# Kernel tuning notes

Measured on AMD Instinct MI355X. Metric: run time of the kernel, lower is better.

Reference implementation:

```python
import jax, jax.numpy as jnp
import numpy as np
from jax import lax

DECAY = 0.1
THRESH = 0.5
LENS = 1.0
D_IN = 2 * 34 * 34  # 2312
HID = 800
NC = 10

@jax.custom_vjp
def act_fun(x):
    return (x > THRESH).astype(x.dtype)

def _act_fwd(x):
    return act_fun(x), x

def _act_bwd(x, g):
    p = jax.nn.sigmoid((x - THRESH) / LENS)
    return (g * p * (1.0 - p) / LENS,)

act_fun.defvjp(_act_fwd, _act_bwd)


def setup_inputs() -> dict:
    key = jax.random.key(0)
    ks = jax.random.split(key, 8)
    B, T = 128, 300
    inp = jax.random.uniform(ks[0], (B, 2, 34, 34, 50), dtype=jnp.float32)
    X = jnp.zeros((B, 2, 34, 34, T), dtype=jnp.float32)
    idx = jax.random.randint(ks[1], (B,), 0, T - 50)
    W1 = jax.random.normal(ks[2], (HID, D_IN), dtype=jnp.float32) * 0.02
    b1 = jnp.zeros((HID,), dtype=jnp.float32)
    W2 = jax.random.normal(ks[3], (NC, HID), dtype=jnp.float32) * 0.03
    b2 = jnp.zeros((NC,), dtype=jnp.float32)
    Wc = jax.random.uniform(ks[4], (1, HID + 4), dtype=jnp.float32)  # ctrl init U(0,1)
    bc = jax.random.uniform(ks[5], (1,), dtype=jnp.float32)
    return {"input": inp, "X": X, "idx": idx, "W1": W1, "b1": b1,
            "W2": W2, "b2": b2, "Wc": Wc, "bc": bc}


def _paste(Xi, clip_i, idx_i):
    # X[i, :, :, :, idx:idx+50] = input[i].view(2,34,34,50)
    return lax.dynamic_update_slice(Xi, clip_i, (0, 0, 0, idx_i))


def reference(input, X, idx, W1, b1, W2, b2, Wc, bc):
    B = X.shape[0]
    T = X.shape[-1]
    X = jax.vmap(_paste)(X, input, idx.astype(jnp.int32))
    xs = jnp.moveaxis(X.reshape(B, D_IN, T), -1, 0)  # [T, B, D_IN]

    t = jnp.arange(T)
    freqs = jnp.stack([
        jnp.ones(T), (t % 2 == 0).astype(jnp.float32),
        (t % 10 == 0).astype(jnp.float32), (t % 100 == 0).astype(jnp.float32),
    ], axis=1).astype(X.dtype)  # [T, 4]
    is_first = (t == 0)

    f32 = X.dtype
    carry0 = (
        jnp.zeros((B, HID), f32), jnp.zeros((B, HID), f32),   # h1_mem, h1_spike
        jnp.zeros((B, NC), f32), jnp.zeros((B, NC), f32),     # h2_mem, h2_spike
        jnp.zeros((B, 1), f32), jnp.zeros((B, 1), f32),       # c_mem, c_spike
        jnp.ones((B, 1), f32), jnp.zeros((B, NC), f32),       # bgt, h2_sumspike
    )

    def step(carry, inps):
        h1m, h1s, h2m, h2s, cm, cs, bgt, sum2 = carry
        x, fq, first = inps
        x_a = jnp.where(first, x, x * cs)
        bgt = jnp.where(cs == 1.0, bgt + 1.0, bgt)
        h1m = h1m * DECAY * (1.0 - h1s) + x_a @ W1.T + b1
        h1s = act_fun(h1m)
        h2m = h2m * DECAY * (1.0 - h2s) + h1s @ W2.T + b2
        h2s = act_fun(h2m)
        c_in = jnp.concatenate(
            [lax.stop_gradient(h1s), jnp.broadcast_to(fq, (B, 4))], axis=1)
        cm = cm * 0.1 * (1.0 - cs) + c_in @ Wc.T + bc
        cs = act_fun(cm)
        sum2 = sum2 + h2s
        return (h1m, h1s, h2m, h2s, cm, cs, bgt, sum2), None

    carry, _ = lax.scan(step, carry0, (xs, freqs, is_first))
    bgt, sum2 = carry[6], carry[7]
    rate = sum2 / bgt
    return rate, X
```

## Files before the change

### kernel.cpp

```cpp
#include <hip/hip_runtime.h>

#define D_IN 2312
#define HID  800
#define NCLS 10
#define BATCH 128
#define TSTEPS 300
#define WIN  50

#define MT 64
#define NT 32
#define BKK 16
#define NTM 100
#define NTN 25
#define GEMM_BLOCKS (NTM * NTN)
#define BLK 128
#define RPASTE 1920
#define TOTQ (BATCH * D_IN * (TSTEPS / 4))

__global__ __launch_bounds__(BLK) void gemm_kernel(
    const float* __restrict__ inp,
    const float* __restrict__ W1,
    float*       __restrict__ P)
{
  __shared__ float As[BKK][MT];
  __shared__ float Bs[BKK][NT + 4];

  int t   = threadIdx.x;
  int bx0 = blockIdx.x;

  int xcd = bx0 & 7;
  int jj  = bx0 >> 3;
  const int q8 = GEMM_BLOCKS >> 3;
  const int r8 = GEMM_BLOCKS & 7;
  int bx = (xcd < r8 ? xcd * (q8 + 1) : r8 * (q8 + 1) + (xcd - r8) * q8) + jj;

  int mt = bx / NTN;
  int nt = bx - mt * NTN;
  int m0 = mt * MT, n0 = nt * NT;

  int am = t & 63;
  int ah = t >> 6;
  int r  = m0 + am;
  int bb = r / 50, ss = r - bb * 50;
  const float* aptr = inp + (size_t)bb * (D_IN * WIN) + ss;

  int bn = t >> 4;
  int bk = t & 15;

  int l  = t & 63;
  int lm = l & 7;
  int ln = l >> 3;
  int tm = ah * 32 + lm * 4;
  int tn = ln * 4;

  float aN[8], bN[4];
#pragma unroll
  for (int q = 0; q < 8; ++q) aN[q] = aptr[(ah * 8 + q) * WIN];
#pragma unroll
  for (int p = 0; p < 4; ++p)
    bN[p] = W1[(size_t)(n0 + bn + 8 * p) * D_IN + bk];

  float acc[4][4] = {};

  for (int k0 = 0; k0 < D_IN; k0 += BKK) {
#pragma unroll
    for (int q = 0; q < 8; ++q) As[ah * 8 + q][am] = aN[q];
#pragma unroll
    for (int p = 0; p < 4; ++p) Bs[bk][bn + 8 * p] = bN[p];
    __syncthreads();

    int kn0 = k0 + BKK;
    if (kn0 + BKK <= D_IN) {
#pragma unroll
      for (int q = 0; q < 8; ++q) aN[q] = aptr[(kn0 + ah * 8 + q) * WIN];
#pragma unroll
      for (int p = 0; p < 4; ++p)
        bN[p] = W1[(size_t)(n0 + bn + 8 * p) * D_IN + kn0 + bk];
    } else if (kn0 < D_IN) {
#pragma unroll
      for (int q = 0; q < 8; ++q) {
        int kk = kn0 + ah * 8 + q;
        aN[q] = (kk < D_IN) ? aptr[kk * WIN] : 0.f;
      }
#pragma unroll
      for (int p = 0; p < 4; ++p) {
        int kk = kn0 + bk;
        bN[p] = (kk < D_IN) ? W1[(size_t)(n0 + bn + 8 * p) * D_IN + kk] : 0.f;
      }
    }

#pragma unroll
    for (int kk = 0; kk < BKK; ++kk) {
      float4 A0 = *(const float4*)&As[kk][tm];
      float4 B0 = *(const float4*)&Bs[kk][tn];
      float av[4] = {A0.x, A0.y, A0.z, A0.w};
      float bv[4] = {B0.x, B0.y, B0.z, B0.w};
#pragma unroll
      for (int i = 0; i < 4; ++i)
#pragma unroll
        for (int j = 0; j < 4; ++j)
          acc[i][j] += av[i] * bv[j];
    }
    __syncthreads();
  }

#pragma unroll
  for (int i = 0; i < 4; ++i) {
    int row = m0 + tm + i;
    *(float4*)&P[(size_t)row * HID + n0 + tn] =
        make_float4(acc[i][0], acc[i][1], acc[i][2], acc[i][3]);
  }
}

template <int CTRL>
__device__ __forceinline__ float dpp_add(float s) {
  return s + __int_as_float(__builtin_amdgcn_update_dpp(
      0, __float_as_int(s), CTRL, 0xf, 0xf, true));
}
__device__ __forceinline__ float wave_sum(float s) {
  s = dpp_add<0x111>(s);
  s = dpp_add<0x112>(s);
  s = dpp_add<0x114>(s);
  s = dpp_add<0x118>(s);
  s = dpp_add<0x142>(s);
  s = dpp_add<0x143>(s);
  return __int_as_float(__builtin_amdgcn_readlane(__float_as_int(s), 63));
}

__global__ __launch_bounds__(64, 1) void recur_kernel(
    const float* __restrict__ P,
    const float* __restrict__ W2,
    const float* __restrict__ b2,
    const float* __restrict__ Wc,
    const float* __restrict__ bc,
    const float* __restrict__ b1,
    const int*   __restrict__ idx,
    float*       __restrict__ out,
    const float* __restrict__ inp,
    float*       __restrict__ outX)
{
  int L = threadIdx.x;
  int b = blockIdx.x;

  if (b >= BATCH) {
    int tid = (b - BATCH) * 64 + L;
    const int stride = RPASTE * 64;
    for (int i = tid; i < TOTQ; i += stride) {
      int q  = i % 75;
      int rd = i / 75;
      int bb = rd / D_IN;
      int d  = rd - bb * D_IN;
      int ib = idx[bb];
      const float* ip = inp + (size_t)bb * (D_IN * WIN) + (size_t)d * WIN;
      int t0 = q * 4;
      float v[4];
#pragma unroll
      for (int e = 0; e < 4; ++e) {
        unsigned w = (unsigned)(t0 + e - ib);
        v[e] = (w < (unsigned)WIN) ? ip[w] : 0.f;
      }
      *(float4*)&outX[(size_t)rd * TSTEPS + t0] = make_float4(v[0], v[1], v[2], v[3]);
    }
    return;
  }

  int myidx = idx[b];
  const float* Pb = P + (size_t)b * WIN * HID;

  float m[13], b1r[13], wcr[13];
  float w2r[NCLS][13];
  unsigned smask = 0;
#pragma unroll
  for (int rr = 0; rr < 13; ++rr) {
    int j = L + 64 * rr;
    bool ok = (j < HID);
    m[rr]   = 0.f;
    b1r[rr] = ok ? b1[j] : 0.f;
    wcr[rr] = ok ? Wc[j] : 0.f;
#pragma unroll
    for (int c = 0; c < NCLS; ++c)
      w2r[c][rr] = ok ? W2[c * HID + j] : 0.f;
  }

  float cm = 0.f, cs = 0.f, bgt = 1.f;
  float bc0 = bc[0];
  float wf0 = Wc[HID], wf1 = Wc[HID + 1], wf2 = Wc[HID + 2], wf3 = Wc[HID + 3];

  float h2m[10], h2s[10], sum2[10], b2r[10];
#pragma unroll
  for (int c = 0; c < NCLS; ++c) { h2m[c] = 0.f; h2s[c] = 0.f; sum2[c] = 0.f; b2r[c] = b2[c]; }

  float cur[13];
  {
    unsigned w0 = (unsigned)(0 - myidx);
    if (w0 < (unsigned)WIN) {
      const float* Pr = Pb + (size_t)w0 * HID;
#pragma unroll
      for (int rr = 0; rr < 13; ++rr) {
        int j = L + 64 * rr;
        cur[rr] = (j < HID) ? Pr[j] : 0.f;
      }
    } else {
#pragma unroll
      for (int rr = 0; rr < 13; ++rr) cur[rr] = 0.f;
    }
  }

  for (int step = 0; step < TSTEPS; ++step) {
    float gate = (step == 0) ? 1.f : cs;

    float nxt[13];
    {
      unsigned wn = (unsigned)(step + 1 - myidx);
      if (wn < (unsigned)WIN) {
        const float* Pr = Pb + (size_t)wn * HID;
#pragma unroll
        for (int rr = 0; rr < 13; ++rr) {
          int j = L + 64 * rr;
          nxt[rr] = (j < HID) ? Pr[j] : 0.f;
        }
      } else {
#pragma unroll
        for (int rr = 0; rr < 13; ++rr) nxt[rr] = 0.f;
      }
    }

    unsigned nmask = 0;
#pragma unroll
    for (int rr = 0; rr < 13; ++rr) {
      float mprev = ((smask >> rr) & 1u) ? 0.f : m[rr] * 0.1f;
      float mv = mprev + cur[rr] * gate + b1r[rr];
      m[rr] = mv;
      nmask |= (mv > 0.5f) ? (1u << rr) : 0u;
    }
    smask = nmask;

    unsigned long long ball = __ballot(smask != 0u);

    float ctrl = 0.f;
    float dot[10];
#pragma unroll
    for (int c = 0; c < NCLS; ++c) dot[c] = 0.f;

    if (ball) {
      float cacc = 0.f;
#pragma unroll
      for (int rr = 0; rr < 13; ++rr) {
        float f = (float)((smask >> rr) & 1u);
        cacc = fmaf(f, wcr[rr], cacc);
      }
      ctrl = wave_sum(cacc);

#pragma unroll
      for (int rr = 0; rr < 13; ++rr) {
        float f = (float)((smask >> rr) & 1u);
#pragma unroll
        for (int c = 0; c < NCLS; ++c)
          dot[c] = fmaf(f, w2r[c][rr], dot[c]);
      }
#pragma unroll
      for (int c = 0; c < NCLS; ++c) dot[c] = wave_sum(dot[c]);
    }

    bgt += (cs == 1.f) ? 1.f : 0.f;
    float fq = wf0;
    if ((step & 1) == 0)   fq += wf1;
    if (step % 10 == 0)    fq += wf2;
    if (step % 100 == 0)   fq += wf3;
    float cv = (cs != 0.f ? 0.f : cm * 0.1f) + ctrl + fq + bc0;
    cm = cv;
    cs = (cv > 0.5f) ? 1.f : 0.f;

#pragma unroll
    for (int c = 0; c < NCLS; ++c) {
      float v = (h2s[c] != 0.f ? 0.f : h2m[c] * 0.1f) + dot[c] + b2r[c];
      h2m[c] = v;
      h2s[c] = (v > 0.5f) ? 1.f : 0.f;
      sum2[c] += h2s[c];
    }

#pragma unroll
    for (int rr = 0; rr < 13; ++rr) cur[rr] = nxt[rr];
  }

  if (L == 0) {
#pragma unroll
    for (int c = 0; c < NCLS; ++c) out[b * NCLS + c] = sum2[c] / bgt;
  }
}

extern "C" void kernel_launch(void* const* d_in, const int* in_sizes, int n_in,
                              void* d_out, int out_size, void* d_ws, size_t ws_size,
                              hipStream_t stream) {
  const float* inp = (const float*)d_in[0];
  const int*   idx = (const int*)d_in[2];
  const float* W1  = (const float*)d_in[3];
  const float* b1  = (const float*)d_in[4];
  const float* W2  = (const float*)d_in[5];
  const float* b2  = (const float*)d_in[6];
  const float* Wc  = (const float*)d_in[7];
  const float* bc  = (const float*)d_in[8];

  float* out = (float*)d_out;
  float* P   = (float*)d_ws;

  gemm_kernel<<<GEMM_BLOCKS, BLK, 0, stream>>>(inp, W1, P);

  recur_kernel<<<BATCH + RPASTE, 64, 0, stream>>>(
      P, W2, b2, Wc, bc, b1, idx, out, inp, out + BATCH * NCLS);
}
```

Before: 1.015 ms.

## Fuse GEMM, recurrence and paste into one kernel with per-tile completion counters

Merges the W1 GEMM, the per-batch spiking recurrence and the X paste into one launch. GEMM blocks bump a per-M-tile atomic counter when done, and each recurrence block spin-waits only on the tiles covering its 50 rows, so recurrence can start before the whole GEMM finishes and the paste overlaps both. The recurrence blocks now read W2 from global memory each step instead of holding it in registers, presumably to cut register pressure under the shared 128-thread launch bound. This risks deadlock if waiting blocks starve GEMM blocks of slots, adds per-step W2 load traffic, and needs extra workspace for the counters, with the old two-kernel path kept as a fallback.

```diff
diff --git a/kernel.cpp b/kernel.cpp
--- a/kernel.cpp
+++ b/kernel.cpp
@@ -14,103 +14,11 @@
 #define NTN 25
 #define GEMM_BLOCKS (NTM * NTN)
 #define BLK 128
-#define RPASTE 1920
+#define RPASTE 960
+#define PASTE_BASE (GEMM_BLOCKS + BATCH)
+#define NB (PASTE_BASE + RPASTE)
 #define TOTQ (BATCH * D_IN * (TSTEPS / 4))
-
-__global__ __launch_bounds__(BLK) void gemm_kernel(
-    const float* __restrict__ inp,
-    const float* __restrict__ W1,
-    float*       __restrict__ P)
-{
-  __shared__ float As[BKK][MT];
-  __shared__ float Bs[BKK][NT + 4];
-
-  int t   = threadIdx.x;
-  int bx0 = blockIdx.x;
-
-  int xcd = bx0 & 7;
-  int jj  = bx0 >> 3;
-  const int q8 = GEMM_BLOCKS >> 3;
-  const int r8 = GEMM_BLOCKS & 7;
-  int bx = (xcd < r8 ? xcd * (q8 + 1) : r8 * (q8 + 1) + (xcd - r8) * q8) + jj;
-
-  int mt = bx / NTN;
-  int nt = bx - mt * NTN;
-  int m0 = mt * MT, n0 = nt * NT;
-
-  int am = t & 63;
-  int ah = t >> 6;
-  int r  = m0 + am;
-  int bb = r / 50, ss = r - bb * 50;
-  const float* aptr = inp + (size_t)bb * (D_IN * WIN) + ss;
-
-  int bn = t >> 4;
-  int bk = t & 15;
-
-  int l  = t & 63;
-  int lm = l & 7;
-  int ln = l >> 3;
-  int tm = ah * 32 + lm * 4;
-  int tn = ln * 4;
-
-  float aN[8], bN[4];
-#pragma unroll
-  for (int q = 0; q < 8; ++q) aN[q] = aptr[(ah * 8 + q) * WIN];
-#pragma unroll
-  for (int p = 0; p < 4; ++p)
-    bN[p] = W1[(size_t)(n0 + bn + 8 * p) * D_IN + bk];
-
-  float acc[4][4] = {};
-
-  for (int k0 = 0; k0 < D_IN; k0 += BKK) {
-#pragma unroll
-    for (int q = 0; q < 8; ++q) As[ah * 8 + q][am] = aN[q];
-#pragma unroll
-    for (int p = 0; p < 4; ++p) Bs[bk][bn + 8 * p] = bN[p];
-    __syncthreads();
-
-    int kn0 = k0 + BKK;
-    if (kn0 + BKK <= D_IN) {
-#pragma unroll
-      for (int q = 0; q < 8; ++q) aN[q] = aptr[(kn0 + ah * 8 + q) * WIN];
-#pragma unroll
-      for (int p = 0; p < 4; ++p)
-        bN[p] = W1[(size_t)(n0 + bn + 8 * p) * D_IN + kn0 + bk];
-    } else if (kn0 < D_IN) {
-#pragma unroll
-      for (int q = 0; q < 8; ++q) {
-        int kk = kn0 + ah * 8 + q;
-        aN[q] = (kk < D_IN) ? aptr[kk * WIN] : 0.f;
-      }
-#pragma unroll
-      for (int p = 0; p < 4; ++p) {
-        int kk = kn0 + bk;
-        bN[p] = (kk < D_IN) ? W1[(size_t)(n0 + bn + 8 * p) * D_IN + kk] : 0.f;
-      }
-    }
-
-#pragma unroll
-    for (int kk = 0; kk < BKK; ++kk) {
-      float4 A0 = *(const float4*)&As[kk][tm];
-      float4 B0 = *(const float4*)&Bs[kk][tn];
-      float av[4] = {A0.x, A0.y, A0.z, A0.w};
-      float bv[4] = {B0.x, B0.y, B0.z, B0.w};
-#pragma unroll
-      for (int i = 0; i < 4; ++i)
-#pragma unroll
-        for (int j = 0; j < 4; ++j)
-          acc[i][j] += av[i] * bv[j];
-    }
-    __syncthreads();
-  }
-
-#pragma unroll
-  for (int i = 0; i < 4; ++i) {
-    int row = m0 + tm + i;
-    *(float4*)&P[(size_t)row * HID + n0 + tn] =
-        make_float4(acc[i][0], acc[i][1], acc[i][2], acc[i][3]);
-  }
-}
+#define P_BYTES (6400 * 800 * 4)
 
 template <int CTRL>
 __device__ __forceinline__ float dpp_add(float s) {
@@ -127,24 +35,391 @@
   return __int_as_float(__builtin_amdgcn_readlane(__float_as_int(s), 63));
 }
 
-__global__ __launch_bounds__(64, 1) void recur_kernel(
-    const float* __restrict__ P,
+__global__ __launch_bounds__(BLK) void fused_all(
+    const float* __restrict__ inp,
+    const float* __restrict__ W1,
+    const int*   __restrict__ idx,
+    float*       __restrict__ P,
     const float* __restrict__ W2,
     const float* __restrict__ b2,
     const float* __restrict__ Wc,
     const float* __restrict__ bc,
     const float* __restrict__ b1,
-    const int*   __restrict__ idx,
     float*       __restrict__ out,
-    const float* __restrict__ inp,
-    float*       __restrict__ outX)
+    float*       __restrict__ outX,
+    int*         __restrict__ cnt)
+{
+  __shared__ float As[BKK][MT];
+  __shared__ float Bs[BKK][NT + 4];
+
+  int t   = threadIdx.x;
+  int bxg = blockIdx.x;
+
+  if (bxg < GEMM_BLOCKS) {
+    int xcd = bxg & 7;
+    int jj  = bxg >> 3;
+    const int q8 = GEMM_BLOCKS >> 3;
+    const int r8 = GEMM_BLOCKS & 7;
+    int bx = (xcd < r8 ? xcd * (q8 + 1) : r8 * (q8 + 1) + (xcd - r8) * q8) + jj;
+
+    int mt = bx / NTN;
+    int nt = bx - mt * NTN;
+    int m0 = mt * MT, n0 = nt * NT;
+
+    int am = t & 63;
+    int ah = t >> 6;
+    int r  = m0 + am;
+    int bb = r / 50, ss = r - bb * 50;
+    const float* aptr = inp + (size_t)bb * (D_IN * WIN) + ss;
+
+    int bn = t >> 4;
+    int bk = t & 15;
+
+    int l  = t & 63;
+    int lm = l & 7;
+    int ln = l >> 3;
+    int tm = ah * 32 + lm * 4;
+    int tn = ln * 4;
+
+    float aN[8], bN[4];
+#pragma unroll
+    for (int q = 0; q < 8; ++q) aN[q] = aptr[(ah * 8 + q) * WIN];
+#pragma unroll
+    for (int p = 0; p < 4; ++p)
+      bN[p] = W1[(size_t)(n0 + bn + 8 * p) * D_IN + bk];
+
+    float acc[4][4] = {};
+
+    for (int k0 = 0; k0 < D_IN; k0 += BKK) {
+#pragma unroll
+      for (int q = 0; q < 8; ++q) As[ah * 8 + q][am] = aN[q];
+#pragma unroll
+      for (int p = 0; p < 4; ++p) Bs[bk][bn + 8 * p] = bN[p];
+      __syncthreads();
+
+      int kn0 = k0 + BKK;
+      if (kn0 + BKK <= D_IN) {
+#pragma unroll
+        for (int q = 0; q < 8; ++q) aN[q] = aptr[(kn0 + ah * 8 + q) * WIN];
+#pragma unroll
+        for (int p = 0; p < 4; ++p)
+          bN[p] = W1[(size_t)(n0 + bn + 8 * p) * D_IN + kn0 + bk];
+      } else if (kn0 < D_IN) {
+#pragma unroll
+        for (int q = 0; q < 8; ++q) {
+          int kk = kn0 + ah * 8 + q;
+          aN[q] = (kk < D_IN) ? aptr[kk * WIN] : 0.f;
+        }
+#pragma unroll
+        for (int p = 0; p < 4; ++p) {
+          int kk = kn0 + bk;
+          bN[p] = (kk < D_IN) ? W1[(size_t)(n0 + bn + 8 * p) * D_IN + kk] : 0.f;
+        }
+      }
+
+#pragma unroll
+      for (int kk = 0; kk < BKK; ++kk) {
+        float4 A0 = *(const float4*)&As[kk][tm];
+        float4 B0 = *(const float4*)&Bs[kk][tn];
+        float av[4] = {A0.x, A0.y, A0.z, A0.w};
+        float bv[4] = {B0.x, B0.y, B0.z, B0.w};
+#pragma unroll
+        for (int i = 0; i < 4; ++i)
+#pragma unroll
+          for (int j = 0; j < 4; ++j)
+            acc[i][j] += av[i] * bv[j];
+      }
+      __syncthreads();
+    }
+
+#pragma unroll
+    for (int i = 0; i < 4; ++i) {
+      int row = m0 + tm + i;
+      *(float4*)&P[(size_t)row * HID + n0 + tn] =
+          make_float4(acc[i][0], acc[i][1], acc[i][2], acc[i][3]);
+    }
+    __syncthreads();
+    if (t == 0) {
+      __threadfence();
+      atomicAdd(&cnt[mt], 1);
+    }
+    return;
+  }
+
+  if (bxg < PASTE_BASE) {
+    if (t >= 64) return;
+    int L = t;
+    int b = bxg - GEMM_BLOCKS;
+
+    int myidx = idx[b];
+    const float* Pb = P + (size_t)b * WIN * HID;
+
+    float m[13], b1r[13], wcr[13];
+    unsigned smask = 0;
+#pragma unroll
+    for (int rr = 0; rr < 13; ++rr) {
+      int j = L + 64 * rr;
+      bool ok = (j < HID);
+      m[rr]   = 0.f;
+      b1r[rr] = ok ? b1[j] : 0.f;
+      wcr[rr] = ok ? Wc[j] : 0.f;
+    }
+
+    float cm = 0.f, cs = 0.f, bgt = 1.f;
+    float bc0 = bc[0];
+    float wf0 = Wc[HID], wf1 = Wc[HID + 1], wf2 = Wc[HID + 2], wf3 = Wc[HID + 3];
+
+    float h2m[10], h2s[10], sum2[10], b2r[10];
+#pragma unroll
+    for (int c = 0; c < NCLS; ++c) { h2m[c] = 0.f; h2s[c] = 0.f; sum2[c] = 0.f; b2r[c] = b2[c]; }
+
+    int mt0 = (50 * b) >> 6;
+    int mt1 = (50 * b + 49) >> 6;
+    for (;;) {
+      int v = __builtin_amdgcn_readfirstlane(atomicAdd(&cnt[mt0], 0));
+      if (v >= NTN) break;
+      __builtin_amdgcn_s_sleep(32);
+    }
+    if (mt1 != mt0) {
+      for (;;) {
+        int v = __builtin_amdgcn_readfirstlane(atomicAdd(&cnt[mt1], 0));
+        if (v >= NTN) break;
+        __builtin_amdgcn_s_sleep(32);
+      }
+    }
+    __threadfence();
+
+    float cur[13];
+    {
+      unsigned w0 = (unsigned)(0 - myidx);
+      if (w0 < (unsigned)WIN) {
+        const float* Pr = Pb + (size_t)w0 * HID;
+#pragma unroll
+        for (int rr = 0; rr < 13; ++rr) {
+          int j = L + 64 * rr;
+          cur[rr] = (j < HID) ? Pr[j] : 0.f;
+        }
+      } else {
+#pragma unroll
+        for (int rr = 0; rr < 13; ++rr) cur[rr] = 0.f;
+      }
+    }
+
+    for (int step = 0; step < TSTEPS; ++step) {
+      float gate = (step == 0) ? 1.f : cs;
+
+      float nxt[13];
+      {
+        unsigned wn = (unsigned)(step + 1 - myidx);
+        if (wn < (unsigned)WIN) {
+          const float* Pr = Pb + (size_t)wn * HID;
+#pragma unroll
+          for (int rr = 0; rr < 13; ++rr) {
+            int j = L + 64 * rr;
+            nxt[rr] = (j < HID) ? Pr[j] : 0.f;
+          }
+        } else {
+#pragma unroll
+          for (int rr = 0; rr < 13; ++rr) nxt[rr] = 0.f;
+        }
+      }
+
+      unsigned nmask = 0;
+#pragma unroll
+      for (int rr = 0; rr < 13; ++rr) {
+        float mprev = ((smask >> rr) & 1u) ? 0.f : m[rr] * 0.1f;
+        float mv = mprev + cur[rr] * gate + b1r[rr];
+        m[rr] = mv;
+        nmask |= (mv > 0.5f) ? (1u << rr) : 0u;
+      }
+      smask = nmask;
+
+      unsigned long long ball = __ballot(smask != 0u);
+
+      float ctrl = 0.f;
+      float dot[10];
+#pragma unroll
+      for (int c = 0; c < NCLS; ++c) dot[c] = 0.f;
+
+      if (ball) {
+        float cacc = 0.f;
+#pragma unroll
+        for (int rr = 0; rr < 13; ++rr) {
+          float f = (float)((smask >> rr) & 1u);
+          cacc = fmaf(f, wcr[rr], cacc);
+        }
+        ctrl = wave_sum(cacc);
+
+#pragma unroll
+        for (int rr = 0; rr < 13; ++rr) {
+          float f = (float)((smask >> rr) & 1u);
+          int j = L + 64 * rr;
+          bool ok = (j < HID);
+#pragma unroll
+          for (int c = 0; c < NCLS; ++c) {
+            float w = ok ? W2[c * HID + j] : 0.f;
+            dot[c] = fmaf(f, w, dot[c]);
+          }
+        }
+#pragma unroll
+        for (int c = 0; c < NCLS; ++c) dot[c] = wave_sum(dot[c]);
+      }
+
+      bgt += (cs == 1.f) ? 1.f : 0.f;
+      float fq = wf0;
+      if ((step & 1) == 0)   fq += wf1;
+      if (step % 10 == 0)    fq += wf2;
+      if (step % 100 == 0)   fq += wf3;
+      float cv = (cs != 0.f ? 0.f : cm * 0.1f) + ctrl + fq + bc0;
+      cm = cv;
+      cs = (cv > 0.5f) ? 1.f : 0.f;
+
+#pragma unroll
+      for (int c = 0; c < NCLS; ++c) {
+        float v = (h2s[c] != 0.f ? 0.f : h2m[c] * 0.1f) + dot[c] + b2r[c];
+        h2m[c] = v;
+        h2s[c] = (v > 0.5f) ? 1.f : 0.f;
+        sum2[c] += h2s[c];
+      }
+
+#pragma unroll
+      for (int rr = 0; rr < 13; ++rr) cur[rr] = nxt[rr];
+    }
+
+    if (L == 0) {
+#pragma unroll
+      for (int c = 0; c < NCLS; ++c) out[b * NCLS + c] = sum2[c] / bgt;
+    }
+    return;
+  }
+
+  {
+    int tid = (bxg - PASTE_BASE) * BLK + t;
+    const int stride = RPASTE * BLK;
+    for (int i = tid; i < TOTQ; i += stride) {
+      int q  = i % 75;
+      int rd = i / 75;
+      int bb = rd / D_IN;
+      int d  = rd - bb * D_IN;
+      int ib = idx[bb];
+      const float* ip = inp + (size_t)bb * (D_IN * WIN) + (size_t)d * WIN;
+      int t0 = q * 4;
+      float v[4];
+#pragma unroll
+      for (int e = 0; e < 4; ++e) {
+        unsigned w = (unsigned)(t0 + e - ib);
+        v[e] = (w < (unsigned)WIN) ? ip[w] : 0.f;
+      }
+      *(float4*)&outX[(size_t)rd * TSTEPS + t0] = make_float4(v[0], v[1], v[2], v[3]);
+    }
+  }
+}
+
+__global__ __launch_bounds__(BLK) void gemm_kernel(
+    const float* __restrict__ inp, const float* __restrict__ W1,
+    float* __restrict__ P)
+{
+  __shared__ float As[BKK][MT];
+  __shared__ float Bs[BKK][NT + 4];
+
+  int t = threadIdx.x;
+  int bx0 = blockIdx.x;
+  int xcd = bx0 & 7;
+  int jj  = bx0 >> 3;
+  const int q8 = GEMM_BLOCKS >> 3;
+  const int r8 = GEMM_BLOCKS & 7;
+  int bx = (xcd < r8 ? xcd * (q8 + 1) : r8 * (q8 + 1) + (xcd - r8) * q8) + jj;
+
+  int mt = bx / NTN;
+  int nt = bx - mt * NTN;
+  int m0 = mt * MT, n0 = nt * NT;
+
+  int am = t & 63;
+  int ah = t >> 6;
+  int r  = m0 + am;
+  int bb = r / 50, ss = r - bb * 50;
+  const float* aptr = inp + (size_t)bb * (D_IN * WIN) + ss;
+
+  int bn = t >> 4;
+  int bk = t & 15;
+  int l  = t & 63;
+  int lm = l & 7;
+  int ln = l >> 3;
+  int tm = ah * 32 + lm * 4;
+  int tn = ln * 4;
+
+  float aN[8], bN[4];
+#pragma unroll
+  for (int q = 0; q < 8; ++q) aN[q] = aptr[(ah * 8 + q) * WIN];
+#pragma unroll
+  for (int p = 0; p < 4; ++p)
+    bN[p] = W1[(size_t)(n0 + bn + 8 * p) * D_IN + bk];
+
+  float acc[4][4] = {};
+
+  for (int k0 = 0; k0 < D_IN; k0 += BKK) {
+#pragma unroll
+    for (int q = 0; q < 8; ++q) As[ah * 8 + q][am] = aN[q];
+#pragma unroll
+    for (int p = 0; p < 4; ++p) Bs[bk][bn + 8 * p] = bN[p];
+    __syncthreads();
+
+    int kn0 = k0 + BKK;
+    if (kn0 + BKK <= D_IN) {
+#pragma unroll
+      for (int q = 0; q < 8; ++q) aN[q] = aptr[(kn0 + ah * 8 + q) * WIN];
+#pragma unroll
+      for (int p = 0; p < 4; ++p)
+        bN[p] = W1[(size_t)(n0 + bn + 8 * p) * D_IN + kn0 + bk];
+    } else if (kn0 < D_IN) {
+#pragma unroll
+      for (int q = 0; q < 8; ++q) {
+        int kk = kn0 + ah * 8 + q;
+        aN[q] = (kk < D_IN) ? aptr[kk * WIN] : 0.f;
+      }
+#pragma unroll
+      for (int p = 0; p < 4; ++p) {
+        int kk = kn0 + bk;
+        bN[p] = (kk < D_IN) ? W1[(size_t)(n0 + bn + 8 * p) * D_IN + kk] : 0.f;
+      }
+    }
+
+#pragma unroll
+    for (int kk = 0; kk < BKK; ++kk) {
+      float4 A0 = *(const float4*)&As[kk][tm];
+      float4 B0 = *(const float4*)&Bs[kk][tn];
+      float av[4] = {A0.x, A0.y, A0.z, A0.w};
+      float bv[4] = {B0.x, B0.y, B0.z, B0.w};
+#pragma unroll
+      for (int i = 0; i < 4; ++i)
+#pragma unroll
+        for (int j = 0; j < 4; ++j)
+          acc[i][j] += av[i] * bv[j];
+    }
+    __syncthreads();
+  }
+
+#pragma unroll
+  for (int i = 0; i < 4; ++i) {
+    int row = m0 + tm + i;
+    *(float4*)&P[(size_t)row * HID + n0 + tn] =
+        make_float4(acc[i][0], acc[i][1], acc[i][2], acc[i][3]);
+  }
+}
+
+__global__ __launch_bounds__(64, 1) void recur_kernel(
+    const float* __restrict__ P, const float* __restrict__ W2,
+    const float* __restrict__ b2, const float* __restrict__ Wc,
+    const float* __restrict__ bc, const float* __restrict__ b1,
+    const int* __restrict__ idx, float* __restrict__ out,
+    const float* __restrict__ inp, float* __restrict__ outX)
 {
   int L = threadIdx.x;
   int b = blockIdx.x;
 
   if (b >= BATCH) {
     int tid = (b - BATCH) * 64 + L;
-    const int stride = RPASTE * 64;
+    const int stride = 1920 * 64;
     for (int i = tid; i < TOTQ; i += stride) {
       int q  = i % 75;
       int rd = i / 75;
@@ -301,11 +576,18 @@
   const float* Wc  = (const float*)d_in[7];
   const float* bc  = (const float*)d_in[8];
 
-  float* out = (float*)d_out;
-  float* P   = (float*)d_ws;
-
-  gemm_kernel<<<GEMM_BLOCKS, BLK, 0, stream>>>(inp, W1, P);
-
-  recur_kernel<<<BATCH + RPASTE, 64, 0, stream>>>(
-      P, W2, b2, Wc, bc, b1, idx, out, inp, out + BATCH * NCLS);
+  float* out  = (float*)d_out;
+  float* P    = (float*)d_ws;
+  float* outX = out + BATCH * NCLS;
+
+  if (ws_size >= (size_t)P_BYTES + NTM * sizeof(int)) {
+    int* cnt = (int*)((char*)d_ws + P_BYTES);
+    hipMemsetAsync(cnt, 0, NTM * sizeof(int), stream);
+    fused_all<<<NB, BLK, 0, stream>>>(
+        inp, W1, idx, P, W2, b2, Wc, bc, b1, out, outX, cnt);
+  } else {
+    gemm_kernel<<<GEMM_BLOCKS, BLK, 0, stream>>>(inp, W1, P);
+    recur_kernel<<<BATCH + 1920, 64, 0, stream>>>(
+        P, W2, b2, Wc, bc, b1, idx, out, inp, outX);
+  }
 }
```

Result: slower. 1.333 ms (+31.4%).
